# Optimization experiments

Hardware: AMD Instinct MI355X
Metric: run time of the kernel (lower is better)

## Reference

```python
import math
import jax, jax.numpy as jnp
import numpy as np

B, S, D_MODEL = 2, 4096, 1024
N_HEADS, D_KV = 16, 64
INNER = N_HEADS * D_KV
BLOCK_LEN = 128          # local_radius(127) + 1
GLOBAL_BLOCK = 16
NUM_BUCKETS, MAX_DIST = 32, 128
EPS = 1e-6
NEG = -1e10


def _rel_bucket(rp):
    # T5 bidirectional relative position bucketing
    nb = NUM_BUCKETS // 2
    buckets = jnp.where(rp > 0, nb, 0).astype(jnp.int32)
    rp = jnp.abs(rp)
    max_exact = nb // 2
    is_small = rp < max_exact
    rp_f = jnp.maximum(rp, 1).astype(jnp.float32)
    rp_large = max_exact + (jnp.log(rp_f / max_exact) / math.log(MAX_DIST / max_exact) * (nb - max_exact)).astype(jnp.int32)
    rp_large = jnp.minimum(rp_large, nb - 1)
    return buckets + jnp.where(is_small, rp.astype(jnp.int32), rp_large)


def _concat3(x, block_dim, seq_dim):
    # concatenate [prev, self, next] blocks along seq_dim (zero-padded at edges)
    nblk = x.shape[block_dim]
    pad = [(0, 0)] * x.ndim
    pad[block_dim] = (1, 1)
    xp = jnp.pad(x, pad)
    blocks = [jax.lax.slice_in_dim(xp, i, i + nblk, axis=block_dim) for i in range(3)]
    return jnp.concatenate(blocks, axis=seq_dim)


def _global_block_ids(mask):
    # faithful port of _make_global_fixed_block_ids
    b, s = mask.shape
    fixed = jnp.cumsum(jnp.full_like(mask, 1.0 / GLOBAL_BLOCK), axis=1) - 1.0 / GLOBAL_BLOCK
    m = jnp.where(mask != 0.0, 1.0, -1000.0).astype(mask.dtype)
    gids = jnp.floor(m + fixed - 1.0)
    gids = jnp.maximum(gids, -1.0)
    gids = gids * mask + (mask - 1.0)
    block_ends = (jnp.arange(s) % GLOBAL_BLOCK) == GLOBAL_BLOCK - 1
    true_ends = jnp.logical_and(block_ends[None, :], gids >= 0)
    full_blocks = true_ends.sum(-1, keepdims=True).astype(gids.dtype) - 1.0
    gids = jnp.where(gids < full_blocks, gids, full_blocks)
    ng = s // GLOBAL_BLOCK
    seq_max = jnp.max(gids, axis=-1, keepdims=True)
    gseg = jnp.where(jnp.arange(ng)[None, :] <= seq_max, 1, 0)
    return gids.astype(jnp.int32), gseg.astype(jnp.int32)


def setup_inputs() -> dict:
    key = jax.random.key(0)
    ks = jax.random.split(key, 8)
    sc = D_MODEL ** -0.5
    return {
        "hidden_states": jax.random.normal(ks[0], (B, S, D_MODEL), jnp.float32),
        "mask": jnp.ones((B, S), jnp.float32),
        "Wq": jax.random.normal(ks[1], (D_MODEL, INNER), jnp.float32) * sc,
        "Wk": jax.random.normal(ks[2], (D_MODEL, INNER), jnp.float32) * sc,
        "Wv": jax.random.normal(ks[3], (D_MODEL, INNER), jnp.float32) * sc,
        "Wo": jax.random.normal(ks[4], (INNER, D_MODEL), jnp.float32) * sc,
        "rel_bias": jax.random.normal(ks[5], (NUM_BUCKETS, N_HEADS), jnp.float32),
        "global_rel_bias": jax.random.normal(ks[6], (NUM_BUCKETS, N_HEADS), jnp.float32),
        "ln_weight": jnp.ones((D_MODEL,), jnp.float32),
    }


def reference(hidden_states, mask, Wq, Wk, Wv, Wo, rel_bias, global_rel_bias, ln_weight):
    b, s, _ = hidden_states.shape
    nb = s // BLOCK_LEN

    gids, gseg = _global_block_ids(mask)
    gsl = gseg.shape[-1]  # global_seq_len

    # global aggregates: sum tokens into their fixed global block (pad ids -1 dropped)
    ids = jnp.where(gids >= 0, gids, gsl)
    one_hot = jax.nn.one_hot(ids, gsl + 1, dtype=hidden_states.dtype)[..., :-1]  # (b,s,g)
    global_inputs = jnp.einsum("bnd,bng->bgd", hidden_states, one_hot)
    # LongT5 RMS layernorm (no mean subtraction, no bias)
    var = jnp.mean(global_inputs.astype(jnp.float32) ** 2, axis=-1, keepdims=True)
    global_inputs = ln_weight * (global_inputs * jax.lax.rsqrt(var + EPS))

    heads = lambda x: x.reshape(x.shape[0], x.shape[1], N_HEADS, D_KV)
    q = heads(hidden_states @ Wq).reshape(b, nb, BLOCK_LEN, N_HEADS, D_KV)
    k = heads(hidden_states @ Wk).reshape(b, nb, BLOCK_LEN, N_HEADS, D_KV)
    v = heads(hidden_states @ Wv).reshape(b, nb, BLOCK_LEN, N_HEADS, D_KV)
    side_k = heads(global_inputs @ Wk)  # (b,g,H,dkv)
    side_v = heads(global_inputs @ Wv)

    k3 = _concat3(k, 1, 2)  # (b,nb,3L,H,dkv)
    v3 = _concat3(v, 1, 2)
    side_k = jnp.broadcast_to(side_k[:, None], (b, nb, gsl, N_HEADS, D_KV))
    side_v = jnp.broadcast_to(side_v[:, None], (b, nb, gsl, N_HEADS, D_KV))
    kk = jnp.concatenate([k3, side_k], axis=2)  # (b,nb,3L+g,H,dkv)
    vv = jnp.concatenate([v3, side_v], axis=2)

    # T5-style: no 1/sqrt(d) scaling
    scores = jnp.einsum("bnqhd,bnkhd->bnhqk", q, kk)  # (b,nb,H,L,3L+g)

    # local relative position bias (1,1,H,L,3L)
    mem_pos = jnp.arange(3 * BLOCK_LEN)
    rel_pos = mem_pos[None, :] - mem_pos[BLOCK_LEN:-BLOCK_LEN][:, None]  # (L,3L)
    local_bias = jnp.transpose(rel_bias[_rel_bucket(rel_pos)], (2, 0, 1))[None, None]

    # local attention mask with locality constraint -> (b,nb,1,L,3L)
    bm = mask.reshape(b, nb, BLOCK_LEN)
    bm3 = _concat3(bm, 1, 2)  # (b,nb,3L)
    lam = (bm[..., None] != 0) & (bm3[..., None, :] != 0)  # (b,nb,L,3L)
    lam = lam & (jnp.abs(rel_pos) < BLOCK_LEN)[None, None]
    local_bias = local_bias + jnp.where(lam[:, :, None], 0.0, NEG)  # (b,nb,H,L,3L)

    # side (local->global) bias: mask + relative bias, (b,H,s,g)
    side_mask = mask[:, :, None] == gseg[:, None, :].astype(mask.dtype)
    side_bias = jnp.where(side_mask, 0.0, NEG)[:, None]  # (b,1,s,g)
    side_rel = jnp.arange(gsl)[None, None, :] - gids[:, :, None]  # (b,s,g)
    side_bias = side_bias + jnp.transpose(global_rel_bias[_rel_bucket(side_rel)], (0, 3, 1, 2))
    # -> (b,nb,H,L,g)
    side_bias = side_bias.reshape(b, N_HEADS, nb, BLOCK_LEN, gsl).transpose(0, 2, 1, 3, 4)

    pos_bias = jnp.concatenate([jnp.broadcast_to(local_bias, scores[..., :3 * BLOCK_LEN].shape), side_bias], axis=-1)

    attn = jax.nn.softmax(scores + pos_bias, axis=-1)
    out = jnp.einsum("bnhqk,bnkhd->bnqhd", attn, vv).reshape(b, s, INNER)
    return out[:, :s] @ Wo
```

## Files before the change

### kernel.cpp

```cpp
#include <hip/hip_runtime.h>

typedef _Float16 h16;
typedef __attribute__((ext_vector_type(4))) _Float16 h16x4;
typedef __attribute__((ext_vector_type(8))) _Float16 h16x8;
typedef __attribute__((ext_vector_type(4))) float f32x4;

#define G_AS __attribute__((address_space(1)))
#define L_AS __attribute__((address_space(3)))

__device__ __forceinline__ void gload_lds16(const void* g, void* l) {
  __builtin_amdgcn_global_load_lds((G_AS void*)(void*)g, (L_AS void*)l, 16, 0, 0);
}

__device__ __forceinline__ f32x4 mfma16(h16x8 a, h16x8 b, f32x4 c) {
  return __builtin_amdgcn_mfma_f32_16x16x32_f16(a, b, c, 0, 0, 0);
}

__global__ __launch_bounds__(256) void fused_prep(const float* __restrict__ hs,
                                                  const float* __restrict__ lnw,
                                                  h16* __restrict__ Xb,
                                                  h16* __restrict__ G) {
  const int bg = blockIdx.x;
  const int t = threadIdx.x;
  const float* base = hs + (long)bg * 16384 + t * 4;
  h16* xout = Xb + (long)bg * 16384 + t * 4;
  float s0 = 0, s1 = 0, s2 = 0, s3 = 0;
#pragma unroll
  for (int r = 0; r < 16; ++r) {
    float4 x = *(const float4*)(base + r * 1024);
    s0 += x.x; s1 += x.y; s2 += x.z; s3 += x.w;
    h16x4 v;
    v[0] = (h16)x.x; v[1] = (h16)x.y; v[2] = (h16)x.z; v[3] = (h16)x.w;
    *(h16x4*)(xout + r * 1024) = v;
  }
  float ss = s0 * s0 + s1 * s1 + s2 * s2 + s3 * s3;
#pragma unroll
  for (int msk = 1; msk < 64; msk <<= 1) ss += __shfl_xor(ss, msk);
  __shared__ float red[4];
  if ((t & 63) == 0) red[t >> 6] = ss;
  __syncthreads();
  float tot = red[0] + red[1] + red[2] + red[3];
  float scale = rsqrtf(tot * (1.f / 1024.f) + 1e-6f);
  float4 lw = *(const float4*)(lnw + t * 4);
  h16* o = G + (long)bg * 1024 + t * 4;
  o[0] = (h16)(s0 * scale * lw.x);
  o[1] = (h16)(s1 * scale * lw.y);
  o[2] = (h16)(s2 * scale * lw.z);
  o[3] = (h16)(s3 * scale * lw.w);
}

__global__ void transpose_w4(const float* __restrict__ s0, const float* __restrict__ s1,
                             const float* __restrict__ s2, const float* __restrict__ s3,
                             h16* __restrict__ d0, h16* __restrict__ d1,
                             h16* __restrict__ d2, h16* __restrict__ d3) {
  const float* src = blockIdx.z == 0 ? s0 : blockIdx.z == 1 ? s1 : blockIdx.z == 2 ? s2 : s3;
  h16* dst = blockIdx.z == 0 ? d0 : blockIdx.z == 1 ? d1 : blockIdx.z == 2 ? d2 : d3;
  __shared__ float t[32][33];
  int bx = blockIdx.x * 32, by = blockIdx.y * 32;
  int tx = threadIdx.x, ty = threadIdx.y;
#pragma unroll
  for (int j = 0; j < 32; j += 8)
    t[ty + j][tx] = src[(long)(by + ty + j) * 1024 + bx + tx];
  __syncthreads();
#pragma unroll
  for (int j = 0; j < 32; j += 8)
    dst[(long)(bx + ty + j) * 1024 + by + tx] = (h16)t[tx][ty + j];
}

__device__ __forceinline__ int bucket_of(int rp) {
  int bb = rp > 0 ? 16 : 0;
  int a = rp < 0 ? -rp : rp;
  if (a < 8) return bb + a;
  int n = 31 - __clz(a * a);
  int idx = 8 + (n - 6);
  idx = idx > 15 ? 15 : idx;
  return bb + idx;
}

__global__ void make_tables(const float* __restrict__ rb, const float* __restrict__ grb,
                            float* __restrict__ LT, float* __restrict__ ST) {
  int i = blockIdx.x * 256 + threadIdx.x;
  if (i >= 16 * 511) return;
  int h = i / 511, r = i % 511;
  int rel = r - 255;
  int bkt = bucket_of(rel);
  int a = rel < 0 ? -rel : rel;
  LT[i] = (a <= 127) ? rb[bkt * 16 + h] : -1e10f;
  ST[i] = grb[bkt * 16 + h];
}

template <int OUTF>
__global__ __launch_bounds__(256) void gemm_bt(const h16* __restrict__ A,
                                               const h16* __restrict__ BT,
                                               void* __restrict__ Cout,
                                               int K, int ldc) {
  __shared__ __align__(16) char As[16384];
  __shared__ __align__(16) char Bs[16384];
  const int tid = threadIdx.x;
  const int lane = tid & 63, w = tid >> 6;
  const int l15 = lane & 15, l16 = lane >> 4;
  const long m0 = (long)blockIdx.y * 128;
  const long n0 = (long)blockIdx.x * 128;
  const char* Ab = (const char*)(A + m0 * K);
  const char* Bb = (const char*)(BT + n0 * K);
  const int wr = w >> 1, wc = w & 1;
  const int srow = w * 32 + (lane >> 3);
  const int spk = (lane & 7) * 16;

  f32x4 acc[4][4] = {};
  for (int kt = 0; kt < K; kt += 64) {
#pragma unroll
    for (int i = 0; i < 4; ++i) {
      int row = srow + i * 8;
      int gk = spk ^ ((row & 7) << 4);
      long goff = (long)row * (K * 2) + kt * 2 + gk;
      gload_lds16(Ab + goff, As + (w * 4 + i) * 1024);
      gload_lds16(Bb + goff, Bs + (w * 4 + i) * 1024);
    }
    __syncthreads();
#pragma unroll
    for (int ks = 0; ks < 2; ++ks) {
      h16x8 af[4], bfv[4];
      int kb = ks * 64 + l16 * 16;
#pragma unroll
      for (int i = 0; i < 4; ++i) {
        int ra = wr * 64 + i * 16 + l15;
        af[i] = *(const h16x8*)(As + ra * 128 + (kb ^ ((ra & 7) << 4)));
        int rb2 = wc * 64 + i * 16 + l15;
        bfv[i] = *(const h16x8*)(Bs + rb2 * 128 + (kb ^ ((rb2 & 7) << 4)));
      }
#pragma unroll
      for (int i = 0; i < 4; ++i)
#pragma unroll
        for (int j = 0; j < 4; ++j)
          acc[i][j] = mfma16(af[i], bfv[j], acc[i][j]);
    }
    __syncthreads();
  }
#pragma unroll
  for (int i = 0; i < 4; ++i)
#pragma unroll
    for (int j = 0; j < 4; ++j)
#pragma unroll
      for (int r = 0; r < 4; ++r) {
        long row = m0 + wr * 64 + i * 16 + l16 * 4 + r;
        long col = n0 + wc * 64 + j * 16 + l15;
        if (OUTF == 0)
          ((h16*)Cout)[row * ldc + col] = (h16)acc[i][j][r];
        else
          ((float*)Cout)[row * ldc + col] = acc[i][j][r];
      }
}

__global__ __launch_bounds__(256, 4) void attn_kernel(
    const h16* __restrict__ QKS, const h16* __restrict__ VtX,
    const float* __restrict__ LT, const float* __restrict__ ST,
    h16* __restrict__ AO) {
  __shared__ float lt[512], st[512];
  __shared__ __align__(16) char pbuf[4][4096];
  const int bid = blockIdx.x;
  const int h = bid & 15, blk = (bid >> 4) & 31, b = bid >> 9;
  const int tid = threadIdx.x, lane = tid & 63, w = tid >> 6;
  const int l15 = lane & 15, l16 = lane >> 4;
  const float L2E = 1.44269504f;

  for (int i = tid; i < 511; i += 256) {
    lt[i] = LT[h * 511 + i];
    st[i] = ST[h * 511 + i];
  }
  __syncthreads();

  const int qb = blk * 128;
  const int qw = qb + w * 32;
  const long tok0 = (long)b * 4096;

  h16x8 qf[2][2];
#pragma unroll
  for (int i = 0; i < 2; ++i)
#pragma unroll
    for (int ks = 0; ks < 2; ++ks)
      qf[i][ks] = *(const h16x8*)(QKS + (tok0 + qw + i * 16 + l15) * 2048 +
                                  h * 64 + ks * 32 + l16 * 8);

  f32x4 o[2][4] = {};
  f32x4 lsum[2] = {};
  float m[2] = {-1e30f, -1e30f};
  char* pb = pbuf[w];

  h16x8 ones;
#pragma unroll
  for (int e = 0; e < 8; ++e) ones[e] = (h16)1.f;

  for (int ci = 0; ci < 10; ++ci) {
    const bool isLocal = ci < 6;
    const int t0 = qb - 128 + ci * 64;
    const int g0 = (ci - 6) * 64;
    if (isLocal && (t0 < 0 || t0 >= 4096)) continue;
    const long krow0 = isLocal ? (tok0 + t0) : (long)(8192 + b * 256 + g0);
    const long vcol0 = isLocal ? (tok0 + t0) : (long)(8192 + b * 256 + g0);

    f32x4 s[2][4];
#pragma unroll
    for (int j = 0; j < 4; ++j) {
      const h16* kp = QKS + (krow0 + j * 16 + l15) * 2048 + 1024 + h * 64 + l16 * 8;
      h16x8 k0 = *(const h16x8*)kp;
      h16x8 k1 = *(const h16x8*)(kp + 32);
#pragma unroll
      for (int i = 0; i < 2; ++i) {
        f32x4 z = {};
        z = mfma16(k0, qf[i][0], z);
        z = mfma16(k1, qf[i][1], z);
        s[i][j] = z;
      }
    }

    float mx[2];
#pragma unroll
    for (int i = 0; i < 2; ++i) {
      const float* tbl = isLocal ? lt : st;
      int bbase = isLocal ? (t0 + l16 * 4 - (qw + i * 16 + l15) + 255)
                          : (g0 + l16 * 4 - ((qw + i * 16 + l15) >> 4) + 255);
      float mj[4];
#pragma unroll
      for (int j = 0; j < 4; ++j) {
#pragma unroll
        for (int r = 0; r < 4; ++r)
          s[i][j][r] += tbl[bbase + j * 16 + r];
        mj[j] = fmaxf(fmaxf(s[i][j][0], s[i][j][1]), fmaxf(s[i][j][2], s[i][j][3]));
      }
      float mm = fmaxf(fmaxf(mj[0], mj[1]), fmaxf(mj[2], mj[3]));
      mm = fmaxf(mm, __shfl_xor(mm, 16));
      mm = fmaxf(mm, __shfl_xor(mm, 32));
      mx[i] = mm;
    }

    bool up = (mx[0] > m[0] + 10.f) || (mx[1] > m[1] + 10.f);
    if (__any(up)) {
#pragma unroll
      for (int i = 0; i < 2; ++i) {
        float mn = mx[i] > m[i] + 10.f ? mx[i] : m[i];
        float al = __builtin_amdgcn_exp2f((m[i] - mn) * L2E);
        m[i] = mn;
#pragma unroll
        for (int r = 0; r < 4; ++r) {
          float ar = __shfl(al, l16 * 4 + r);
          lsum[i][r] *= ar;
#pragma unroll
          for (int df = 0; df < 4; ++df) o[i][df][r] *= ar;
        }
      }
    }

#pragma unroll
    for (int i = 0; i < 2; ++i) {
      float mi = m[i];
      int q = i * 16 + l15;
      int x = (q & 7) << 4;
      int base = q * 128 + ((l16 * 8) ^ (x & 0x10));
      int xr = x & 0x60;
#pragma unroll
      for (int j = 0; j < 4; ++j) {
        h16x4 ph;
#pragma unroll
        for (int r = 0; r < 4; ++r)
          ph[r] = (h16)__builtin_amdgcn_exp2f((s[i][j][r] - mi) * L2E);
        *(h16x4*)(pb + base + ((j * 32) ^ xr)) = ph;
      }
    }

#pragma unroll
    for (int ks = 0; ks < 2; ++ks) {
      h16x8 pa[2];
#pragma unroll
      for (int i = 0; i < 2; ++i) {
        int q = i * 16 + l15;
        int x = (q & 7) << 4;
        int rb2 = q * 128 + ((l16 * 16) ^ (x & 0x30)) + ((ks * 64) ^ (x & 0x40));
        pa[i] = *(const h16x8*)(pb + rb2);
      }
      h16x8 vf[4];
#pragma unroll
      for (int df = 0; df < 4; ++df)
        vf[df] = *(const h16x8*)(VtX + (long)(h * 64 + df * 16 + l15) * 8704 +
                                 vcol0 + ks * 32 + l16 * 8);
#pragma unroll
      for (int i = 0; i < 2; ++i) {
        lsum[i] = mfma16(pa[i], ones, lsum[i]);
#pragma unroll
        for (int df = 0; df < 4; ++df)
          o[i][df] = mfma16(pa[i], vf[df], o[i][df]);
      }
    }
  }

#pragma unroll
  for (int i = 0; i < 2; ++i) {
#pragma unroll
    for (int r = 0; r < 4; ++r) {
      float inv = 1.f / lsum[i][r];
      long row = tok0 + qw + i * 16 + l16 * 4 + r;
#pragma unroll
      for (int df = 0; df < 4; ++df)
        AO[row * 1024 + h * 64 + df * 16 + l15] = (h16)(o[i][df][r] * inv);
    }
  }
}

extern "C" void kernel_launch(void* const* d_in, const int* in_sizes, int n_in,
                              void* d_out, int out_size, void* d_ws, size_t ws_size,
                              hipStream_t stream) {
  const float* hs = (const float*)d_in[0];
  const float* Wq = (const float*)d_in[2];
  const float* Wk = (const float*)d_in[3];
  const float* Wv = (const float*)d_in[4];
  const float* Wo = (const float*)d_in[5];
  const float* rb = (const float*)d_in[6];
  const float* grb = (const float*)d_in[7];
  const float* lnw = (const float*)d_in[8];

  char* p = (char*)d_ws;
  auto take = [&](size_t bytes) {
    char* r = p;
    p += (bytes + 255) & ~(size_t)255;
    return r;
  };
  h16* Xb   = (h16*)take(8704l * 1024 * 2);
  h16* G    = Xb + 8192l * 1024;
  h16* WqkT = (h16*)take(2048l * 1024 * 2);
  h16* WvT  = (h16*)take(1024l * 1024 * 2);
  h16* WoT  = (h16*)take(1024l * 1024 * 2);
  h16* QKS  = (h16*)take(8704l * 2048 * 2);
  h16* VtX  = (h16*)take(1024l * 8704 * 2);
  h16* AO   = (h16*)take(8192l * 1024 * 2);
  float* LT = (float*)take(16l * 511 * 4);
  float* ST = (float*)take(16l * 511 * 4);

  fused_prep<<<512, 256, 0, stream>>>(hs, lnw, Xb, G);
  transpose_w4<<<dim3(32, 32, 4), dim3(32, 8), 0, stream>>>(
      Wq, Wk, Wv, Wo, WqkT, WqkT + 1024l * 1024, WvT, WoT);
  make_tables<<<32, 256, 0, stream>>>(rb, grb, LT, ST);

  gemm_bt<0><<<dim3(16, 68), 256, 0, stream>>>(Xb, WqkT, QKS, 1024, 2048);
  gemm_bt<0><<<dim3(68, 8), 256, 0, stream>>>(WvT, Xb, VtX, 1024, 8704);

  attn_kernel<<<1024, 256, 0, stream>>>(QKS, VtX, LT, ST, AO);

  gemm_bt<1><<<dim3(8, 64), 256, 0, stream>>>(AO, WoT, d_out, 1024, 1024);
}
```

Measured before the change: 290.0 us.

## Replace GEMMs with 256x256 double-buffered 8-wave pipelined kernel and merge QK/V launches

Replaces the simple 128x128 single-buffered GEMM with a 256x256-tile, 512-thread kernel. It double-buffers 128 KB of LDS and interleaves global-to-LDS staging of the next K tile with four MFMA phases, using barriers and s_setprio. The QK and V projections are fused into one launch by splitting the block index range. The aim is to hide memory latency and cut launch count, at the cost of fewer blocks (408 and 128) and one block per CU, which may underfill the GPU.

```diff
diff --git a/kernel.cpp b/kernel.cpp
--- a/kernel.cpp
+++ b/kernel.cpp
@@ -15,6 +15,13 @@
 __device__ __forceinline__ f32x4 mfma16(h16x8 a, h16x8 b, f32x4 c) {
   return __builtin_amdgcn_mfma_f32_16x16x32_f16(a, b, c, 0, 0, 0);
 }
+
+#define PHASE_BAR()                     \
+  do {                                  \
+    asm volatile("" ::: "memory");      \
+    __builtin_amdgcn_s_barrier();       \
+    asm volatile("" ::: "memory");      \
+  } while (0)
 
 __global__ __launch_bounds__(256) void fused_prep(const float* __restrict__ hs,
                                                   const float* __restrict__ lnw,
@@ -89,66 +96,158 @@
   ST[i] = grb[bkt * 16 + h];
 }
 
+__device__ __forceinline__ void stage_half(const char* g, long ldb, char* ldsb,
+                                           int tid) {
+  const int rw = tid >> 3;
+  const int colb = ((tid & 7) * 16) ^ ((rw & 7) << 4);
+  const int w = tid >> 6;
+  gload_lds16(g + (long)rw * ldb + colb, ldsb + (w * 8) * 128);
+  gload_lds16(g + (long)(rw + 64) * ldb + colb, ldsb + (64 + w * 8) * 128);
+}
+
 template <int OUTF>
-__global__ __launch_bounds__(256) void gemm_bt(const h16* __restrict__ A,
-                                               const h16* __restrict__ BT,
-                                               void* __restrict__ Cout,
-                                               int K, int ldc) {
-  __shared__ __align__(16) char As[16384];
-  __shared__ __align__(16) char Bs[16384];
+__global__ __launch_bounds__(512, 1) void gemm8p(
+    const h16* __restrict__ A0, const h16* __restrict__ B0, void* __restrict__ C0,
+    int ldc0, int nt0, int split,
+    const h16* __restrict__ A1, const h16* __restrict__ B1, void* __restrict__ C1,
+    int ldc1, int nt1, int K) {
+  extern __shared__ char lds[];
   const int tid = threadIdx.x;
   const int lane = tid & 63, w = tid >> 6;
   const int l15 = lane & 15, l16 = lane >> 4;
-  const long m0 = (long)blockIdx.y * 128;
-  const long n0 = (long)blockIdx.x * 128;
-  const char* Ab = (const char*)(A + m0 * K);
-  const char* Bb = (const char*)(BT + n0 * K);
-  const int wr = w >> 1, wc = w & 1;
-  const int srow = w * 32 + (lane >> 3);
-  const int spk = (lane & 7) * 16;
-
-  f32x4 acc[4][4] = {};
-  for (int kt = 0; kt < K; kt += 64) {
-#pragma unroll
-    for (int i = 0; i < 4; ++i) {
-      int row = srow + i * 8;
-      int gk = spk ^ ((row & 7) << 4);
-      long goff = (long)row * (K * 2) + kt * 2 + gk;
-      gload_lds16(Ab + goff, As + (w * 4 + i) * 1024);
-      gload_lds16(Bb + goff, Bs + (w * 4 + i) * 1024);
-    }
-    __syncthreads();
-#pragma unroll
-    for (int ks = 0; ks < 2; ++ks) {
-      h16x8 af[4], bfv[4];
-      int kb = ks * 64 + l16 * 16;
-#pragma unroll
-      for (int i = 0; i < 4; ++i) {
-        int ra = wr * 64 + i * 16 + l15;
-        af[i] = *(const h16x8*)(As + ra * 128 + (kb ^ ((ra & 7) << 4)));
-        int rb2 = wc * 64 + i * 16 + l15;
-        bfv[i] = *(const h16x8*)(Bs + rb2 * 128 + (kb ^ ((rb2 & 7) << 4)));
-      }
-#pragma unroll
-      for (int i = 0; i < 4; ++i)
-#pragma unroll
-        for (int j = 0; j < 4; ++j)
-          acc[i][j] = mfma16(af[i], bfv[j], acc[i][j]);
-    }
-    __syncthreads();
-  }
-#pragma unroll
-  for (int i = 0; i < 4; ++i)
-#pragma unroll
-    for (int j = 0; j < 4; ++j)
+  const int wr = w >> 2, wc = w & 3;
+
+  const h16* A; const h16* BT; char* Cb; int ldc, mt, nt;
+  {
+    int bid = blockIdx.x;
+    if (bid < split) { A = A0; BT = B0; Cb = (char*)C0; ldc = ldc0; mt = bid / nt0; nt = bid % nt0; }
+    else { int b2 = bid - split; A = A1; BT = B1; Cb = (char*)C1; ldc = ldc1; mt = b2 / nt1; nt = b2 % nt1; }
+  }
+  const long m0g = (long)mt * 256, n0g = (long)nt * 256;
+  const long ldb = (long)K * 2;
+  const char* Ag = (const char*)A + m0g * ldb;
+  const char* Bg = (const char*)BT + n0g * ldb;
+  const int nkt = K >> 6;
+
+  char* ALDS = lds;
+  char* BLDS = lds + 65536;
+
+  stage_half(Ag, ldb, ALDS, tid);
+  stage_half(Ag + 128 * ldb, ldb, ALDS + 16384, tid);
+  stage_half(Bg, ldb, BLDS, tid);
+  stage_half(Bg + 128 * ldb, ldb, BLDS + 16384, tid);
+  stage_half(Ag + 128, ldb, ALDS + 32768, tid);
+  stage_half(Ag + 128 * ldb + 128, ldb, ALDS + 32768 + 16384, tid);
+  asm volatile("s_waitcnt vmcnt(4)" ::: "memory");
+  __builtin_amdgcn_s_barrier();
+  asm volatile("" ::: "memory");
+
+  f32x4 acc[8][4] = {};
+  h16x8 af[8][2], bf[4][2];
+
+  const char* aHalfB = ALDS + wr * 16384;
+  const char* bHalfB = BLDS + (wc >> 1) * 16384;
+  const int brow0 = (wc & 1) * 64;
+
+  for (int t = 0; t < nkt; ++t) {
+    const int p = t & 1, q = p ^ 1;
+    const char* aH = aHalfB + p * 32768;
+    const char* bH = bHalfB + p * 32768;
+    const bool s1 = (t + 1) < nkt, s2 = (t + 2) < nkt;
+
+#pragma unroll
+    for (int m = 0; m < 4; ++m) {
+      int r = m * 16 + l15;
+      af[m][0] = *(const h16x8*)(aH + r * 128 + ((l16 * 16) ^ ((r & 7) << 4)));
+      af[m][1] = *(const h16x8*)(aH + r * 128 + ((64 + l16 * 16) ^ ((r & 7) << 4)));
+    }
+#pragma unroll
+    for (int n = 0; n < 2; ++n) {
+      int r = brow0 + n * 16 + l15;
+      bf[n][0] = *(const h16x8*)(bH + r * 128 + ((l16 * 16) ^ ((r & 7) << 4)));
+      bf[n][1] = *(const h16x8*)(bH + r * 128 + ((64 + l16 * 16) ^ ((r & 7) << 4)));
+    }
+    if (s1) stage_half(Bg + (long)(t + 1) * 128, ldb, BLDS + q * 32768, tid);
+    PHASE_BAR();
+    __builtin_amdgcn_s_setprio(1);
+#pragma unroll
+    for (int m = 0; m < 4; ++m)
+#pragma unroll
+      for (int n = 0; n < 2; ++n) {
+        acc[m][n] = mfma16(af[m][0], bf[n][0], acc[m][n]);
+        acc[m][n] = mfma16(af[m][1], bf[n][1], acc[m][n]);
+      }
+    __builtin_amdgcn_s_setprio(0);
+    PHASE_BAR();
+
+#pragma unroll
+    for (int m = 4; m < 8; ++m) {
+      int r = m * 16 + l15;
+      af[m][0] = *(const h16x8*)(aH + r * 128 + ((l16 * 16) ^ ((r & 7) << 4)));
+      af[m][1] = *(const h16x8*)(aH + r * 128 + ((64 + l16 * 16) ^ ((r & 7) << 4)));
+    }
+#pragma unroll
+    for (int n = 2; n < 4; ++n) {
+      int r = brow0 + n * 16 + l15;
+      bf[n][0] = *(const h16x8*)(bH + r * 128 + ((l16 * 16) ^ ((r & 7) << 4)));
+      bf[n][1] = *(const h16x8*)(bH + r * 128 + ((64 + l16 * 16) ^ ((r & 7) << 4)));
+    }
+    if (s1) stage_half(Bg + 128 * ldb + (long)(t + 1) * 128, ldb,
+                       BLDS + q * 32768 + 16384, tid);
+    PHASE_BAR();
+    __builtin_amdgcn_s_setprio(1);
+#pragma unroll
+    for (int m = 4; m < 8; ++m)
+#pragma unroll
+      for (int n = 2; n < 4; ++n) {
+        acc[m][n] = mfma16(af[m][0], bf[n][0], acc[m][n]);
+        acc[m][n] = mfma16(af[m][1], bf[n][1], acc[m][n]);
+      }
+    __builtin_amdgcn_s_setprio(0);
+    PHASE_BAR();
+
+    if (s2) stage_half(Ag + (long)(t + 2) * 128, ldb, ALDS + p * 32768, tid);
+    PHASE_BAR();
+    __builtin_amdgcn_s_setprio(1);
+#pragma unroll
+    for (int m = 0; m < 4; ++m)
+#pragma unroll
+      for (int n = 2; n < 4; ++n) {
+        acc[m][n] = mfma16(af[m][0], bf[n][0], acc[m][n]);
+        acc[m][n] = mfma16(af[m][1], bf[n][1], acc[m][n]);
+      }
+    __builtin_amdgcn_s_setprio(0);
+    PHASE_BAR();
+
+    if (s2) stage_half(Ag + 128 * ldb + (long)(t + 2) * 128, ldb,
+                       ALDS + p * 32768 + 16384, tid);
+    PHASE_BAR();
+    __builtin_amdgcn_s_setprio(1);
+#pragma unroll
+    for (int m = 4; m < 8; ++m)
+#pragma unroll
+      for (int n = 0; n < 2; ++n) {
+        acc[m][n] = mfma16(af[m][0], bf[n][0], acc[m][n]);
+        acc[m][n] = mfma16(af[m][1], bf[n][1], acc[m][n]);
+      }
+    __builtin_amdgcn_s_setprio(0);
+    if (s2) asm volatile("s_waitcnt vmcnt(4)" ::: "memory");
+    else    asm volatile("s_waitcnt vmcnt(0)" ::: "memory");
+    PHASE_BAR();
+  }
+
+#pragma unroll
+  for (int m = 0; m < 8; ++m)
+#pragma unroll
+    for (int n = 0; n < 4; ++n)
 #pragma unroll
       for (int r = 0; r < 4; ++r) {
-        long row = m0 + wr * 64 + i * 16 + l16 * 4 + r;
-        long col = n0 + wc * 64 + j * 16 + l15;
+        long row = m0g + wr * 128 + m * 16 + l16 * 4 + r;
+        long col = n0g + wc * 64 + n * 16 + l15;
         if (OUTF == 0)
-          ((h16*)Cout)[row * ldc + col] = (h16)acc[i][j][r];
+          ((h16*)Cb)[row * ldc + col] = (h16)acc[m][n][r];
         else
-          ((float*)Cout)[row * ldc + col] = acc[i][j][r];
+          ((float*)Cb)[row * ldc + col] = acc[m][n][r];
       }
 }
 
@@ -335,15 +434,27 @@
   float* LT = (float*)take(16l * 511 * 4);
   float* ST = (float*)take(16l * 511 * 4);
 
+  static bool attr_done = false;
+  if (!attr_done) {
+    hipFuncSetAttribute((const void*)gemm8p<0>,
+                        hipFuncAttributeMaxDynamicSharedMemorySize, 131072);
+    hipFuncSetAttribute((const void*)gemm8p<1>,
+                        hipFuncAttributeMaxDynamicSharedMemorySize, 131072);
+    attr_done = true;
+  }
+
   fused_prep<<<512, 256, 0, stream>>>(hs, lnw, Xb, G);
   transpose_w4<<<dim3(32, 32, 4), dim3(32, 8), 0, stream>>>(
       Wq, Wk, Wv, Wo, WqkT, WqkT + 1024l * 1024, WvT, WoT);
   make_tables<<<32, 256, 0, stream>>>(rb, grb, LT, ST);
 
-  gemm_bt<0><<<dim3(16, 68), 256, 0, stream>>>(Xb, WqkT, QKS, 1024, 2048);
-  gemm_bt<0><<<dim3(68, 8), 256, 0, stream>>>(WvT, Xb, VtX, 1024, 8704);
+  gemm8p<0><<<dim3(272 + 136), 512, 131072, stream>>>(
+      Xb, WqkT, QKS, 2048, 8, 272,
+      WvT, Xb, VtX, 8704, 34, 1024);
 
   attn_kernel<<<1024, 256, 0, stream>>>(QKS, VtX, LT, ST, AO);
 
-  gemm_bt<1><<<dim3(8, 64), 256, 0, stream>>>(AO, WoT, d_out, 1024, 1024);
-}
+  gemm8p<1><<<dim3(128), 512, 131072, stream>>>(
+      AO, WoT, d_out, 1024, 4, 128,
+      AO, WoT, d_out, 1024, 4, 1024);
+}
```

Result: no change. 289.1 us (-0.3%).
